# Kernel optimization log

Measured on AMD Instinct MI355X. Metric: run time of the kernel, lower is better.

## Reference

```python
import jax, jax.numpy as jnp
import numpy as np

B, OBS, N, HEADS, SIZE, HID = 8192, 512, 8, 5, 64, 1024
SUM = HEADS * SIZE  # sum(per_robot_dims) = 320
NEG = -1.0e9


def setup_inputs() -> dict:
    key = jax.random.key(0)
    ks = jax.random.split(key, 12)
    init = lambda k, sh, fan: (jax.random.normal(k, sh, jnp.float32) / np.sqrt(fan)).astype(jnp.float32)
    obs = jax.random.normal(ks[0], (B, OBS), jnp.float32)
    actions = jax.random.randint(ks[1], (B, N * HEADS), 0, SIZE)
    masks = jax.random.randint(ks[2], (B, N, HEADS, SIZE), 0, 2).astype(jnp.int32)
    return {
        "obs": obs,
        "actions": actions,
        "masks": masks,
        "W1": init(ks[3], (OBS, HID), OBS), "b1": jnp.zeros((HID,), jnp.float32),
        "W2": init(ks[4], (HID, HID), HID), "b2": jnp.zeros((HID,), jnp.float32),
        "headsW": init(ks[5], (N, HID, SUM), HID), "headsb": jnp.zeros((N, SUM), jnp.float32),
        "Wc1": init(ks[6], (HID, HID // 2), HID), "bc1": jnp.zeros((HID // 2,), jnp.float32),
        "Wc2": init(ks[7], (HID // 2, 1), HID // 2), "bc2": jnp.zeros((1,), jnp.float32),
    }


def reference(obs, actions, masks, W1, b1, W2, b2, headsW, headsb, Wc1, bc1, Wc2, bc2):
    # Shared encoder: two Linear+ReLU layers.
    h = jax.nn.relu(obs @ W1 + b1)
    h = jax.nn.relu(h @ W2 + b2)  # [B, HID]
    # Per-robot heads, batched into one einsum: [B, N, SUM]
    logits = jnp.einsum('bh,nhs->bns', h, headsW) + headsb
    seg = logits.reshape(B, N, HEADS, SIZE)
    # Masked softmax: invalid entries set to -1e9 (matches seg[~mask] = -1e9).
    seg = jnp.where(masks.astype(bool), seg, NEG)
    logp = jax.nn.log_softmax(seg, axis=-1)          # [B, N, HEADS, SIZE]
    probs = jnp.exp(logp)
    acts = actions.reshape(B, N, HEADS)
    lp_terms = jnp.take_along_axis(logp, acts[..., None], axis=-1)[..., 0]
    ent_terms = -jnp.sum(probs * logp, axis=-1)
    # Out-of-range action -> log-prob -1000 and no entropy contribution.
    valid = acts < SIZE
    logps = jnp.where(valid, lp_terms, -1000.0).sum(axis=(1, 2))
    entropy = jnp.where(valid, ent_terms, 0.0).sum(axis=(1, 2))
    # Critic value head.
    values = (jax.nn.relu(h @ Wc1 + bc1) @ Wc2 + bc2)[..., 0]
    return logps, entropy, values
```

## Files before the change

### kernel.cpp

```cpp
#include <hip/hip_runtime.h>
#include <hip/hip_bf16.h>
#include <stdint.h>


typedef __bf16 v8bf __attribute__((ext_vector_type(8)));
typedef float  v4f  __attribute__((ext_vector_type(4)));

__device__ __forceinline__ void load_lds16(const void* g, void* l) {
  auto gp = (const __attribute__((address_space(1))) char*)(uintptr_t)g;
  auto lp = (__attribute__((address_space(3))) char*)(uintptr_t)l;
  __builtin_amdgcn_global_load_lds(gp, lp, 16, 0, 0);
}


__global__ void convert_obs(const float4* __restrict__ in, int4* __restrict__ out, int n8) {
  const int i = blockIdx.x * blockDim.x + threadIdx.x;
  if (i >= n8) return;
  const float4 x = in[i * 2], y = in[i * 2 + 1];
  union { __hip_bfloat16 h[8]; int4 v; } u;
  u.h[0] = __float2bfloat16(x.x);
  u.h[1] = __float2bfloat16(x.y);
  u.h[2] = __float2bfloat16(x.z);
  u.h[3] = __float2bfloat16(x.w);
  u.h[4] = __float2bfloat16(y.x);
  u.h[5] = __float2bfloat16(y.y);
  u.h[6] = __float2bfloat16(y.z);
  u.h[7] = __float2bfloat16(y.w);
  out[i] = u.v;
}

__global__ void build_bias(const float* __restrict__ headsb, const float* __restrict__ bc1,
                           float* __restrict__ biasc) {
  const int i = blockIdx.x * blockDim.x + threadIdx.x;
  if (i < 2560) biasc[i] = headsb[i];
  else if (i < 3072) biasc[i] = bc1[i - 2560];
}

__global__ void transpose_to_bf16(const float* __restrict__ in, __hip_bfloat16* __restrict__ out,
                                  int R, int C) {
  __shared__ float t[32][33];
  const int bx = blockIdx.x * 32, by = blockIdx.y * 32;
  in  += (size_t)blockIdx.z * R * C;
  out += (size_t)blockIdx.z * R * C;
  const int x = threadIdx.x, y = threadIdx.y;
#pragma unroll
  for (int i = 0; i < 32; i += 8)
    t[y + i][x] = in[(size_t)(by + y + i) * C + bx + x];
  __syncthreads();
#pragma unroll
  for (int i = 0; i < 32; i += 8)
    out[(size_t)(bx + y + i) * R + by + x] = __float2bfloat16(t[x][y + i]);
}


__global__ __launch_bounds__(256, 2)
void gemm_bf16_tn(const __hip_bfloat16* __restrict__ A,
                  const __hip_bfloat16* __restrict__ Bt,
                  const float* __restrict__ bias,
                  __hip_bfloat16* __restrict__ C,
                  int M, int N, int K, int relu_from) {
  __shared__ char As[8192];
  __shared__ char Bs[8192];
  const int tid  = threadIdx.x;
  const int lane = tid & 63;
  const int wave = tid >> 6;
  const int wr = wave >> 1, wc = wave & 1;
  const int m0 = blockIdx.y * 128, n0 = blockIdx.x * 128;

  const int c0 = tid, c1 = tid + 256;
  const int r0 = ((c0 >> 3) << 1) | (((c0 >> 2) ^ (c0 >> 4)) & 1);
  const int s0 = (c0 & 3) ^ (r0 & 3);
  const int r1 = ((c1 >> 3) << 1) | (((c1 >> 2) ^ (c1 >> 4)) & 1);
  const int s1 = (c1 & 3) ^ (r1 & 3);

  const char* pa0 = (const char*)A  + ((size_t)(m0 + r0) * K) * 2 + s0 * 16;
  const char* pa1 = (const char*)A  + ((size_t)(m0 + r1) * K) * 2 + s1 * 16;
  const char* pb0 = (const char*)Bt + ((size_t)(n0 + r0) * K) * 2 + s0 * 16;
  const char* pb1 = (const char*)Bt + ((size_t)(n0 + r1) * K) * 2 + s1 * 16;

  char* la0 = As + c0 * 16;
  char* la1 = As + c1 * 16;
  char* lb0 = Bs + c0 * 16;
  char* lb1 = Bs + c1 * 16;

  const int lr = lane & 15, ls = lane >> 4;
  int offA[4], offB[4];
#pragma unroll
  for (int m = 0; m < 4; ++m) {
    const int rA = wr * 64 + m * 16 + lr;
    offA[m] = ((rA * 4 + (ls ^ (rA & 3))) ^ (rA & 4)) * 16;
    const int rB = wc * 64 + m * 16 + lr;
    offB[m] = ((rB * 4 + (ls ^ (rB & 3))) ^ (rB & 4)) * 16;
  }

  v4f acc[4][4] = {};

  const int nk = K >> 5;
  for (int it = 0; it < nk; ++it) {
    load_lds16(pa0, la0);
    load_lds16(pa1, la1);
    load_lds16(pb0, lb0);
    load_lds16(pb1, lb1);
    pa0 += 64; pa1 += 64; pb0 += 64; pb1 += 64;
    __syncthreads();

    v8bf av[4], bvv[4];
#pragma unroll
    for (int m = 0; m < 4; ++m) av[m]  = *(const v8bf*)(As + offA[m]);
#pragma unroll
    for (int n = 0; n < 4; ++n) bvv[n] = *(const v8bf*)(Bs + offB[n]);
#pragma unroll
    for (int m = 0; m < 4; ++m)
#pragma unroll
      for (int n = 0; n < 4; ++n)
        acc[m][n] = __builtin_amdgcn_mfma_f32_16x16x32_bf16(av[m], bvv[n], acc[m][n], 0, 0, 0);
    __syncthreads();
  }

  const int colb = n0 + wc * 64 + lr;
  const int rowb = m0 + wr * 64 + ls * 4;
#pragma unroll
  for (int n = 0; n < 4; ++n) {
    const int col = colb + n * 16;
    const float bv = bias[col];
    const bool rl = (col >= relu_from);
#pragma unroll
    for (int m = 0; m < 4; ++m) {
      const int rbase = rowb + m * 16;
#pragma unroll
      for (int j = 0; j < 4; ++j) {
        float v = acc[m][n][j] + bv;
        if (rl) v = fmaxf(v, 0.0f);
        C[(size_t)(rbase + j) * N + col] = __float2bfloat16(v);
      }
    }
  }
}


__global__ __launch_bounds__(256)
void finalize_kernel(const __hip_bfloat16* __restrict__ out3,
                     const int* __restrict__ masks,
                     const int* __restrict__ actions,
                     const float* __restrict__ Wc2,
                     const float* __restrict__ bc2,
                     float* __restrict__ out) {
  const int lane = threadIdx.x & 63;
  const int r = blockIdx.x * 4 + (threadIdx.x >> 6);
  const __hip_bfloat16* row = out3 + (size_t)r * 3072;
  const int* mrow = masks + (size_t)r * 2560;
  const int* arow = actions + r * 40;

  const int g = lane >> 3;
  const int gl = lane & 7;

  float lp_sum = 0.f, ent_sum = 0.f;

#pragma unroll
  for (int p = 0; p < 5; ++p) {
    const int base = p * 512 + lane * 8;
    union { int4 q; __hip_bfloat16 h[8]; } u;
    u.q = *(const int4*)(row + base);
    const int4 ma = *(const int4*)(mrow + base);
    const int4 mb = *(const int4*)(mrow + base + 4);

    float v[8];
    v[0] = ma.x ? __bfloat162float(u.h[0]) : -1.0e9f;
    v[1] = ma.y ? __bfloat162float(u.h[1]) : -1.0e9f;
    v[2] = ma.z ? __bfloat162float(u.h[2]) : -1.0e9f;
    v[3] = ma.w ? __bfloat162float(u.h[3]) : -1.0e9f;
    v[4] = mb.x ? __bfloat162float(u.h[4]) : -1.0e9f;
    v[5] = mb.y ? __bfloat162float(u.h[5]) : -1.0e9f;
    v[6] = mb.z ? __bfloat162float(u.h[6]) : -1.0e9f;
    v[7] = mb.w ? __bfloat162float(u.h[7]) : -1.0e9f;

    float mx = fmaxf(fmaxf(fmaxf(v[0], v[1]), fmaxf(v[2], v[3])),
                     fmaxf(fmaxf(v[4], v[5]), fmaxf(v[6], v[7])));
#pragma unroll
    for (int o = 1; o < 8; o <<= 1) mx = fmaxf(mx, __shfl_xor(mx, o));

    float s = 0.f, sv = 0.f;
#pragma unroll
    for (int j = 0; j < 8; ++j) {
      const float e = __expf(v[j] - mx);
      s += e;
      sv += e * v[j];
    }
#pragma unroll
    for (int o = 1; o < 8; o <<= 1) { s += __shfl_xor(s, o); sv += __shfl_xor(sv, o); }

    const float logZ = __logf(s) + mx;

    const int act = arow[p * 8 + g];
    float va_loc = v[0];
#pragma unroll
    for (int j = 1; j < 8; ++j) va_loc = ((act & 7) == j) ? v[j] : va_loc;
    const float va = __shfl(va_loc, (lane & 56) | ((act >> 3) & 7));

    if ((unsigned)act < 64u) {
      lp_sum += va - logZ;
      ent_sum += logZ - sv / s;
    } else {
      lp_sum += -1000.0f;
    }
  }

#pragma unroll
  for (int o = 8; o < 64; o <<= 1) {
    lp_sum += __shfl_xor(lp_sum, o);
    ent_sum += __shfl_xor(ent_sum, o);
  }

  union { int4 q; __hip_bfloat16 h[8]; } c;
  c.q = *(const int4*)(row + 2560 + lane * 8);
  const float4 w0 = *(const float4*)(Wc2 + lane * 8);
  const float4 w1 = *(const float4*)(Wc2 + lane * 8 + 4);
  float acc = __bfloat162float(c.h[0]) * w0.x + __bfloat162float(c.h[1]) * w0.y +
              __bfloat162float(c.h[2]) * w0.z + __bfloat162float(c.h[3]) * w0.w +
              __bfloat162float(c.h[4]) * w1.x + __bfloat162float(c.h[5]) * w1.y +
              __bfloat162float(c.h[6]) * w1.z + __bfloat162float(c.h[7]) * w1.w;
#pragma unroll
  for (int o = 32; o > 0; o >>= 1) acc += __shfl_xor(acc, o);

  if (lane == 0) {
    out[r]         = lp_sum;
    out[8192 + r]  = ent_sum;
    out[16384 + r] = acc + bc2[0];
  }
}


extern "C" void kernel_launch(void* const* d_in, const int* in_sizes, int n_in,
                              void* d_out, int out_size, void* d_ws, size_t ws_size,
                              hipStream_t stream) {
  const float* obs    = (const float*)d_in[0];
  const int*   actions= (const int*)d_in[1];
  const int*   masks  = (const int*)d_in[2];
  const float* W1     = (const float*)d_in[3];
  const float* b1     = (const float*)d_in[4];
  const float* W2     = (const float*)d_in[5];
  const float* b2     = (const float*)d_in[6];
  const float* headsW = (const float*)d_in[7];
  const float* headsb = (const float*)d_in[8];
  const float* Wc1    = (const float*)d_in[9];
  const float* bc1    = (const float*)d_in[10];
  const float* Wc2    = (const float*)d_in[11];
  const float* bc2    = (const float*)d_in[12];
  float* out = (float*)d_out;

  char* ws = (char*)d_ws;
  __hip_bfloat16* obsB  = (__hip_bfloat16*)(ws);
  __hip_bfloat16* W1t   = (__hip_bfloat16*)(ws + 8388608);
  __hip_bfloat16* W2t   = (__hip_bfloat16*)(ws + 9437184);
  __hip_bfloat16* Wbigt = (__hip_bfloat16*)(ws + 11534336);
  float*          biasc = (float*)(ws + 17825792);
  __hip_bfloat16* h1    = (__hip_bfloat16*)(ws + 17838080);
  __hip_bfloat16* h2    = (__hip_bfloat16*)(ws + 34615296);
  __hip_bfloat16* out3  = (__hip_bfloat16*)(ws + 51392512);

  convert_obs<<<2048, 256, 0, stream>>>((const float4*)obs, (int4*)obsB, 524288);
  build_bias<<<12, 256, 0, stream>>>(headsb, bc1, biasc);
  transpose_to_bf16<<<dim3(32, 16, 1), dim3(32, 8), 0, stream>>>(W1, W1t, 512, 1024);
  transpose_to_bf16<<<dim3(32, 32, 1), dim3(32, 8), 0, stream>>>(W2, W2t, 1024, 1024);
  transpose_to_bf16<<<dim3(10, 32, 8), dim3(32, 8), 0, stream>>>(headsW, Wbigt, 1024, 320);
  transpose_to_bf16<<<dim3(16, 32, 1), dim3(32, 8), 0, stream>>>(Wc1, Wbigt + 2560 * 1024, 1024, 512);

  gemm_bf16_tn<<<dim3(8, 64), 256, 0, stream>>>(obsB, W1t, b1, h1, 8192, 1024, 512, 0);
  gemm_bf16_tn<<<dim3(8, 64), 256, 0, stream>>>(h1, W2t, b2, h2, 8192, 1024, 1024, 0);
  gemm_bf16_tn<<<dim3(24, 64), 256, 0, stream>>>(h2, Wbigt, biasc, out3, 8192, 3072, 1024, 2560);

  finalize_kernel<<<2048, 256, 0, stream>>>(out3, masks, actions, Wc2, bc2, out);
}
```

Measured before the change: 154.3 us.

## Replace GEMM with 256x256-tile double-buffered 8-phase pipelined kernel

Swaps the simple 128x128, single-buffer, K=32-per-step GEMM for a 512-thread kernel that computes 256x256 output tiles with K=128 steps. Global-to-LDS loads are double buffered and interleaved with MFMA phases using explicit waitcnt, barriers, sched_barrier and setprio. Block IDs are remapped across 8 groups to spread tiles over XCDs. The goal is to hide memory latency and raise data reuse per tile, at the cost of 128KB of LDS, more registers and fewer blocks (128/384), which risks poor CU occupancy on the smaller GEMMs.

```diff
diff --git a/kernel.cpp b/kernel.cpp
--- a/kernel.cpp
+++ b/kernel.cpp
@@ -53,79 +53,190 @@
 }
 
 
-__global__ __launch_bounds__(256, 2)
-void gemm_bf16_tn(const __hip_bfloat16* __restrict__ A,
-                  const __hip_bfloat16* __restrict__ Bt,
-                  const float* __restrict__ bias,
-                  __hip_bfloat16* __restrict__ C,
-                  int M, int N, int K, int relu_from) {
-  __shared__ char As[8192];
-  __shared__ char Bs[8192];
+__device__ __forceinline__ void rd_a(v8bf (&a)[4][2], const char* base, int mbase) {
+#pragma unroll
+  for (int m = 0; m < 4; ++m)
+#pragma unroll
+    for (int ks = 0; ks < 2; ++ks)
+      a[m][ks] = *(const v8bf*)(base + (((mbase + m) * 2 + ks) << 10));
+}
+
+__device__ __forceinline__ void rd_b2(v8bf (&b)[4][2], const char* base, int n0) {
+#pragma unroll
+  for (int n = 0; n < 2; ++n)
+#pragma unroll
+    for (int ks = 0; ks < 2; ++ks)
+      b[n0 + n][ks] = *(const v8bf*)(base + (((n0 + n) * 2 + ks) << 10));
+}
+
+template<int M0, int N0>
+__device__ __forceinline__ void mfma_quad(v4f (&acc)[8][4], const v8bf (&a)[4][2],
+                                          const v8bf (&b)[4][2]) {
+#pragma unroll
+  for (int m = 0; m < 4; ++m)
+#pragma unroll
+    for (int n = 0; n < 2; ++n)
+#pragma unroll
+      for (int ks = 0; ks < 2; ++ks)
+        acc[M0 + m][N0 + n] =
+            __builtin_amdgcn_mfma_f32_16x16x32_bf16(a[m][ks], b[N0 + n][ks],
+                                                    acc[M0 + m][N0 + n], 0, 0, 0);
+}
+
+#define BARRIER __builtin_amdgcn_s_barrier()
+#define SCHEDB  __builtin_amdgcn_sched_barrier(0)
+#define WAIT_LGKM0 do { asm volatile("s_waitcnt lgkmcnt(0)" ::: "memory"); SCHEDB; } while (0)
+#define WAIT_VM2   do { asm volatile("s_waitcnt vmcnt(2)" ::: "memory"); SCHEDB; } while (0)
+#define WAIT_VM0   do { asm volatile("s_waitcnt vmcnt(0)" ::: "memory"); SCHEDB; } while (0)
+
+#define MFMA_PH(Q) do { __builtin_amdgcn_s_setprio(1); Q; __builtin_amdgcn_s_setprio(0); SCHEDB; } while (0)
+
+#define ST_A0(db) { load_lds16(pA0a, s0 + ((db) << 16));          load_lds16(pA0b, s0 + ((db) << 16) + 8192);  pA0a += 128; pA0b += 128; }
+#define ST_A1(db) { load_lds16(pA1a, s0 + ((db) << 16) + 16384);  load_lds16(pA1b, s0 + ((db) << 16) + 24576); pA1a += 128; pA1b += 128; }
+#define ST_B0(db) { load_lds16(pB0a, s0 + ((db) << 16) + 32768);  load_lds16(pB0b, s0 + ((db) << 16) + 40960); pB0a += 128; pB0b += 128; }
+#define ST_B1(db) { load_lds16(pB1a, s0 + ((db) << 16) + 49152);  load_lds16(pB1b, s0 + ((db) << 16) + 57344); pB1a += 128; pB1b += 128; }
+
+__global__ __launch_bounds__(512, 2)
+void gemm_8ph(const __hip_bfloat16* __restrict__ A,
+              const __hip_bfloat16* __restrict__ Bt,
+              const float* __restrict__ bias,
+              __hip_bfloat16* __restrict__ C,
+              int M, int N, int K, int relu_from, int gx) {
+  __shared__ char smem[131072];
+
   const int tid  = threadIdx.x;
   const int lane = tid & 63;
   const int wave = tid >> 6;
-  const int wr = wave >> 1, wc = wave & 1;
-  const int m0 = blockIdx.y * 128, n0 = blockIdx.x * 128;
-
-  const int c0 = tid, c1 = tid + 256;
-  const int r0 = ((c0 >> 3) << 1) | (((c0 >> 2) ^ (c0 >> 4)) & 1);
-  const int s0 = (c0 & 3) ^ (r0 & 3);
-  const int r1 = ((c1 >> 3) << 1) | (((c1 >> 2) ^ (c1 >> 4)) & 1);
-  const int s1 = (c1 & 3) ^ (r1 & 3);
-
-  const char* pa0 = (const char*)A  + ((size_t)(m0 + r0) * K) * 2 + s0 * 16;
-  const char* pa1 = (const char*)A  + ((size_t)(m0 + r1) * K) * 2 + s1 * 16;
-  const char* pb0 = (const char*)Bt + ((size_t)(n0 + r0) * K) * 2 + s0 * 16;
-  const char* pb1 = (const char*)Bt + ((size_t)(n0 + r1) * K) * 2 + s1 * 16;
-
-  char* la0 = As + c0 * 16;
-  char* la1 = As + c1 * 16;
-  char* lb0 = Bs + c0 * 16;
-  char* lb1 = Bs + c1 * 16;
-
+  const int wr = wave >> 2;
+  const int wc = wave & 3;
   const int lr = lane & 15, ls = lane >> 4;
-  int offA[4], offB[4];
-#pragma unroll
-  for (int m = 0; m < 4; ++m) {
-    const int rA = wr * 64 + m * 16 + lr;
-    offA[m] = ((rA * 4 + (ls ^ (rA & 3))) ^ (rA & 4)) * 16;
-    const int rB = wc * 64 + m * 16 + lr;
-    offB[m] = ((rB * 4 + (ls ^ (rB & 3))) ^ (rB & 4)) * 16;
-  }
-
-  v4f acc[4][4] = {};
-
-  const int nk = K >> 5;
-  for (int it = 0; it < nk; ++it) {
-    load_lds16(pa0, la0);
-    load_lds16(pa1, la1);
-    load_lds16(pb0, lb0);
-    load_lds16(pb1, lb1);
-    pa0 += 64; pa1 += 64; pb0 += 64; pb1 += 64;
-    __syncthreads();
-
-    v8bf av[4], bvv[4];
-#pragma unroll
-    for (int m = 0; m < 4; ++m) av[m]  = *(const v8bf*)(As + offA[m]);
-#pragma unroll
-    for (int n = 0; n < 4; ++n) bvv[n] = *(const v8bf*)(Bs + offB[n]);
-#pragma unroll
-    for (int m = 0; m < 4; ++m)
-#pragma unroll
-      for (int n = 0; n < 4; ++n)
-        acc[m][n] = __builtin_amdgcn_mfma_f32_16x16x32_bf16(av[m], bvv[n], acc[m][n], 0, 0, 0);
-    __syncthreads();
-  }
+
+  const int nwg = gridDim.x;
+  const int q8 = nwg >> 3;
+  const int id = (blockIdx.x & 7) * q8 + (blockIdx.x >> 3);
+  const int bx = id % gx, by = id / gx;
+  const int m0 = by * 256, n0 = bx * 256;
+
+  const int o0 = tid << 4;
+  const int s_0 = o0 ^ (((o0 >> 9) & 1) << 5);
+  const int r0 = ((s_0 >> 10) >> 1) * 16 + ((s_0 >> 6) & 15);
+  const int cb0 = (((((s_0 >> 10) & 1) << 2) | ((s_0 >> 4) & 3)) << 4);
+  const int o1 = (tid + 512) << 4;
+  const int s_1 = o1 ^ (((o1 >> 9) & 1) << 5);
+  const int r1 = ((s_1 >> 10) >> 1) * 16 + ((s_1 >> 6) & 15);
+  const int cb1 = (((((s_1 >> 10) & 1) << 2) | ((s_1 >> 4) & 3)) << 4);
+
+  const size_t K2 = (size_t)K * 2;
+  const char* pA0a = (const char*)A + (size_t)(m0 +       r0) * K2 + cb0;
+  const char* pA0b = (const char*)A + (size_t)(m0 +       r1) * K2 + cb1;
+  const char* pA1a = (const char*)A + (size_t)(m0 + 128 + r0) * K2 + cb0;
+  const char* pA1b = (const char*)A + (size_t)(m0 + 128 + r1) * K2 + cb1;
+  const char* pB0a = (const char*)Bt + (size_t)(n0 +       r0) * K2 + cb0;
+  const char* pB0b = (const char*)Bt + (size_t)(n0 +       r1) * K2 + cb1;
+  const char* pB1a = (const char*)Bt + (size_t)(n0 + 128 + r0) * K2 + cb0;
+  const char* pB1b = (const char*)Bt + (size_t)(n0 + 128 + r1) * K2 + cb1;
+
+  char* const s0 = smem + (tid << 4);
+
+  const int laneOff = lr * 64 + ((ls * 16) ^ ((lr & 8) << 2));
+  const char* aB0 = smem + wr * 16384 + laneOff;
+  const char* bB0 = smem + 32768 + (wc >> 1) * 16384 + (wc & 1) * 8192 + laneOff;
+  const char* aB1 = aB0 + 65536;
+  const char* bB1 = bB0 + 65536;
+
+  v4f acc[8][4] = {};
+  v8bf aLo[4][2], aHi[4][2], bFr[4][2];
+
+  ST_A0(0); ST_A1(0); ST_B0(0); ST_B1(0);
+  ST_A0(1);
+  WAIT_VM2;
+  BARRIER; SCHEDB;
+
+  const int NI = (K >> 7) - 1;
+  for (int i = 0; i < NI; ++i) {
+    rd_a(aLo, aB0, 0); rd_b2(bFr, bB0, 0);
+    ST_A1(1);
+    BARRIER; WAIT_LGKM0;
+    MFMA_PH((mfma_quad<0, 0>(acc, aLo, bFr)));
+    BARRIER;
+    rd_b2(bFr, bB0, 2);
+    ST_B0(1);
+    BARRIER; WAIT_LGKM0;
+    MFMA_PH((mfma_quad<0, 2>(acc, aLo, bFr)));
+    BARRIER;
+    rd_a(aHi, aB0, 4);
+    ST_B1(1);
+    BARRIER; WAIT_LGKM0;
+    MFMA_PH((mfma_quad<4, 2>(acc, aHi, bFr)));
+    BARRIER;
+    ST_A0(0);
+    WAIT_VM2;
+    BARRIER;
+    MFMA_PH((mfma_quad<4, 0>(acc, aHi, bFr)));
+    BARRIER;
+    rd_a(aLo, aB1, 0); rd_b2(bFr, bB1, 0);
+    ST_A1(0);
+    BARRIER; WAIT_LGKM0;
+    MFMA_PH((mfma_quad<0, 0>(acc, aLo, bFr)));
+    BARRIER;
+    rd_b2(bFr, bB1, 2);
+    ST_B0(0);
+    BARRIER; WAIT_LGKM0;
+    MFMA_PH((mfma_quad<0, 2>(acc, aLo, bFr)));
+    BARRIER;
+    rd_a(aHi, aB1, 4);
+    ST_B1(0);
+    BARRIER; WAIT_LGKM0;
+    MFMA_PH((mfma_quad<4, 2>(acc, aHi, bFr)));
+    BARRIER;
+    ST_A0(1);
+    WAIT_VM2;
+    BARRIER;
+    MFMA_PH((mfma_quad<4, 0>(acc, aHi, bFr)));
+    BARRIER;
+  }
+
+  rd_a(aLo, aB0, 0); rd_b2(bFr, bB0, 0);
+  ST_A1(1);
+  BARRIER; WAIT_LGKM0;
+  MFMA_PH((mfma_quad<0, 0>(acc, aLo, bFr)));
+  BARRIER;
+  rd_b2(bFr, bB0, 2);
+  ST_B0(1);
+  BARRIER; WAIT_LGKM0;
+  MFMA_PH((mfma_quad<0, 2>(acc, aLo, bFr)));
+  BARRIER;
+  rd_a(aHi, aB0, 4);
+  ST_B1(1);
+  BARRIER; WAIT_LGKM0;
+  MFMA_PH((mfma_quad<4, 2>(acc, aHi, bFr)));
+  BARRIER;
+  WAIT_VM0;
+  BARRIER;
+  MFMA_PH((mfma_quad<4, 0>(acc, aHi, bFr)));
+  BARRIER;
+  rd_a(aLo, aB1, 0); rd_b2(bFr, bB1, 0);
+  BARRIER; WAIT_LGKM0;
+  MFMA_PH((mfma_quad<0, 0>(acc, aLo, bFr)));
+  BARRIER;
+  rd_b2(bFr, bB1, 2);
+  BARRIER; WAIT_LGKM0;
+  MFMA_PH((mfma_quad<0, 2>(acc, aLo, bFr)));
+  BARRIER;
+  rd_a(aHi, aB1, 4);
+  BARRIER; WAIT_LGKM0;
+  MFMA_PH((mfma_quad<4, 2>(acc, aHi, bFr)));
+  MFMA_PH((mfma_quad<4, 0>(acc, aHi, bFr)));
 
   const int colb = n0 + wc * 64 + lr;
-  const int rowb = m0 + wr * 64 + ls * 4;
+  const int rowb = m0 + wr * 128 + ls * 4;
 #pragma unroll
   for (int n = 0; n < 4; ++n) {
     const int col = colb + n * 16;
     const float bv = bias[col];
     const bool rl = (col >= relu_from);
 #pragma unroll
-    for (int m = 0; m < 4; ++m) {
+    for (int m = 0; m < 8; ++m) {
       const int rbase = rowb + m * 16;
 #pragma unroll
       for (int j = 0; j < 4; ++j) {
@@ -152,7 +263,6 @@
   const int* arow = actions + r * 40;
 
   const int g = lane >> 3;
-  const int gl = lane & 7;
 
   float lp_sum = 0.f, ent_sum = 0.f;
 
@@ -265,9 +375,9 @@
   transpose_to_bf16<<<dim3(10, 32, 8), dim3(32, 8), 0, stream>>>(headsW, Wbigt, 1024, 320);
   transpose_to_bf16<<<dim3(16, 32, 1), dim3(32, 8), 0, stream>>>(Wc1, Wbigt + 2560 * 1024, 1024, 512);
 
-  gemm_bf16_tn<<<dim3(8, 64), 256, 0, stream>>>(obsB, W1t, b1, h1, 8192, 1024, 512, 0);
-  gemm_bf16_tn<<<dim3(8, 64), 256, 0, stream>>>(h1, W2t, b2, h2, 8192, 1024, 1024, 0);
-  gemm_bf16_tn<<<dim3(24, 64), 256, 0, stream>>>(h2, Wbigt, biasc, out3, 8192, 3072, 1024, 2560);
+  gemm_8ph<<<dim3(128), 512, 0, stream>>>(obsB, W1t, b1, h1, 8192, 1024, 512, 0, 4);
+  gemm_8ph<<<dim3(128), 512, 0, stream>>>(h1, W2t, b2, h2, 8192, 1024, 1024, 0, 4);
+  gemm_8ph<<<dim3(384), 512, 0, stream>>>(h2, Wbigt, biasc, out3, 8192, 3072, 1024, 2560, 12);
 
   finalize_kernel<<<2048, 256, 0, stream>>>(out3, masks, actions, Wc2, bc2, out);
 }
```

Result: slower. 159.8 us (+3.5%).

## Replace bf16 GEMM with 4-stage pipelined, larger-tile 512-thread kernel

Applied to the files above, without the earlier changes.

Replaces the single-buffered 128x128 GEMM with a templated kernel that uses 256-row tiles, 8 waves, and a 4-deep LDS ring. Global-to-LDS loads are issued several k-steps ahead, with explicit vmcnt and lgkmcnt waits and raw barriers, so memory latency can overlap the MFMA work. It also remaps block IDs across 8 groups to improve cache locality, and raises wave priority around the MFMA bursts. The cost is much larger LDS use per block, which may limit occupancy to one block per CU, and more fragile hand-written synchronisation.

```diff
diff --git a/kernel.cpp b/kernel.cpp
--- a/kernel.cpp
+++ b/kernel.cpp
@@ -10,6 +10,20 @@
   auto gp = (const __attribute__((address_space(1))) char*)(uintptr_t)g;
   auto lp = (__attribute__((address_space(3))) char*)(uintptr_t)l;
   __builtin_amdgcn_global_load_lds(gp, lp, 16, 0, 0);
+}
+
+#define BARRIER __builtin_amdgcn_s_barrier()
+#define SCHEDB  __builtin_amdgcn_sched_barrier(0)
+#define WAIT_LGKM0 do { asm volatile("s_waitcnt lgkmcnt(0)" ::: "memory"); SCHEDB; } while (0)
+
+template<int N>
+__device__ __forceinline__ void wait_vm() {
+  if constexpr (N == 8)      asm volatile("s_waitcnt vmcnt(8)" ::: "memory");
+  else if constexpr (N == 6) asm volatile("s_waitcnt vmcnt(6)" ::: "memory");
+  else if constexpr (N == 4) asm volatile("s_waitcnt vmcnt(4)" ::: "memory");
+  else if constexpr (N == 3) asm volatile("s_waitcnt vmcnt(3)" ::: "memory");
+  else                       asm volatile("s_waitcnt vmcnt(0)" ::: "memory");
+  SCHEDB;
 }
 
 
@@ -53,79 +67,133 @@
 }
 
 
-__global__ __launch_bounds__(256, 2)
-void gemm_bf16_tn(const __hip_bfloat16* __restrict__ A,
-                  const __hip_bfloat16* __restrict__ Bt,
-                  const float* __restrict__ bias,
-                  __hip_bfloat16* __restrict__ C,
-                  int M, int N, int K, int relu_from) {
-  __shared__ char As[8192];
-  __shared__ char Bs[8192];
+__device__ __forceinline__ void decode_chunk(int o, int& r, int& cb) {
+  const int L = o ^ (((o >> 9) & 1) << 5);
+  r  = ((L >> 10) << 4) | ((L >> 6) & 15);
+  cb = ((L >> 4) & 3) << 4;
+}
+
+template<int WM>
+__global__ __launch_bounds__(512, 2)
+void gemm_kt(const __hip_bfloat16* __restrict__ A,
+             const __hip_bfloat16* __restrict__ Bt,
+             const float* __restrict__ bias,
+             __hip_bfloat16* __restrict__ C,
+             int N, int K, int relu_from, int gx) {
+  constexpr int WN   = 8 / WM;
+  constexpr int MR   = 16 / WM;
+  constexpr int BREG = WN * 4096;
+  constexpr int TB   = 16384 + BREG;
+  constexpr int NSTG = 2 + WN / 2;
+
+  __shared__ char smem[4 * TB];
+
   const int tid  = threadIdx.x;
   const int lane = tid & 63;
   const int wave = tid >> 6;
-  const int wr = wave >> 1, wc = wave & 1;
-  const int m0 = blockIdx.y * 128, n0 = blockIdx.x * 128;
-
-  const int c0 = tid, c1 = tid + 256;
-  const int r0 = ((c0 >> 3) << 1) | (((c0 >> 2) ^ (c0 >> 4)) & 1);
-  const int s0 = (c0 & 3) ^ (r0 & 3);
-  const int r1 = ((c1 >> 3) << 1) | (((c1 >> 2) ^ (c1 >> 4)) & 1);
-  const int s1 = (c1 & 3) ^ (r1 & 3);
-
-  const char* pa0 = (const char*)A  + ((size_t)(m0 + r0) * K) * 2 + s0 * 16;
-  const char* pa1 = (const char*)A  + ((size_t)(m0 + r1) * K) * 2 + s1 * 16;
-  const char* pb0 = (const char*)Bt + ((size_t)(n0 + r0) * K) * 2 + s0 * 16;
-  const char* pb1 = (const char*)Bt + ((size_t)(n0 + r1) * K) * 2 + s1 * 16;
-
-  char* la0 = As + c0 * 16;
-  char* la1 = As + c1 * 16;
-  char* lb0 = Bs + c0 * 16;
-  char* lb1 = Bs + c1 * 16;
-
+  const int wr = wave / WN, wc = wave % WN;
   const int lr = lane & 15, ls = lane >> 4;
-  int offA[4], offB[4];
-#pragma unroll
-  for (int m = 0; m < 4; ++m) {
-    const int rA = wr * 64 + m * 16 + lr;
-    offA[m] = ((rA * 4 + (ls ^ (rA & 3))) ^ (rA & 4)) * 16;
-    const int rB = wc * 64 + m * 16 + lr;
-    offB[m] = ((rB * 4 + (ls ^ (rB & 3))) ^ (rB & 4)) * 16;
-  }
-
-  v4f acc[4][4] = {};
-
-  const int nk = K >> 5;
-  for (int it = 0; it < nk; ++it) {
-    load_lds16(pa0, la0);
-    load_lds16(pa1, la1);
-    load_lds16(pb0, lb0);
-    load_lds16(pb1, lb1);
-    pa0 += 64; pa1 += 64; pb0 += 64; pb1 += 64;
-    __syncthreads();
-
-    v8bf av[4], bvv[4];
-#pragma unroll
-    for (int m = 0; m < 4; ++m) av[m]  = *(const v8bf*)(As + offA[m]);
-#pragma unroll
-    for (int n = 0; n < 4; ++n) bvv[n] = *(const v8bf*)(Bs + offB[n]);
+
+  const int nwg = gridDim.x;
+  const int q8 = nwg >> 3;
+  const int id = (blockIdx.x & 7) * q8 + (blockIdx.x >> 3);
+  const int bx = id % gx, by = id / gx;
+  const int m0 = by * 256, n0 = bx * (WN * 64);
+
+  int rA0, cA0, rA1, cA1, rB0, cB0, rB1, cB1;
+  decode_chunk(tid * 16, rA0, cA0);
+  decode_chunk(tid * 16 + 8192, rA1, cA1);
+  decode_chunk(tid * 16, rB0, cB0);
+  decode_chunk(tid * 16 + 8192, rB1, cB1);
+
+  const size_t K2 = (size_t)K * 2;
+  const char* pA0 = (const char*)A + (size_t)(m0 + rA0) * K2 + cA0;
+  const char* pA1 = (const char*)A + (size_t)(m0 + rA1) * K2 + cA1;
+  const char* pB0 = (const char*)Bt + (size_t)(n0 + rB0) * K2 + cB0;
+  const char* pB1 = (const char*)Bt + (size_t)(n0 + rB1) * K2 + cB1;
+
+  char* const s0 = smem + (tid << 4);
+
+  const int laneOff = lr * 64 + ((ls * 16) ^ ((lr & 8) << 2));
+
+  v4f acc[MR][4] = {};
+
+  auto stage_A = [&](int stOff) {
+    load_lds16(pA0, s0 + stOff);
+    load_lds16(pA1, s0 + stOff + 8192);
+    pA0 += 64; pA1 += 64;
+  };
+  auto stage_B = [&](int stOff) {
+    load_lds16(pB0, s0 + stOff + 16384);
+    pB0 += 64;
+    if constexpr (WN == 4) {
+      load_lds16(pB1, s0 + stOff + 24576);
+      pB1 += 64;
+    }
+  };
+
+  auto tile = [&](int bufOff, int stOff, bool doStage, auto gate) {
+    const char* aB = smem + bufOff + wr * (MR * 1024) + laneOff;
+    const char* bB = smem + bufOff + 16384 + wc * 4096 + laneOff;
+    v8bf af[4], bfr[4];
+#pragma unroll
+    for (int m = 0; m < 4; ++m) af[m] = *(const v8bf*)(aB + m * 1024);
+#pragma unroll
+    for (int n = 0; n < 4; ++n) bfr[n] = *(const v8bf*)(bB + n * 1024);
+    if (doStage) {
+      stage_A(stOff);
+      if constexpr (MR == 4) stage_B(stOff);
+    }
+    BARRIER; WAIT_LGKM0;
+    __builtin_amdgcn_s_setprio(1);
 #pragma unroll
     for (int m = 0; m < 4; ++m)
 #pragma unroll
       for (int n = 0; n < 4; ++n)
-        acc[m][n] = __builtin_amdgcn_mfma_f32_16x16x32_bf16(av[m], bvv[n], acc[m][n], 0, 0, 0);
-    __syncthreads();
-  }
+        acc[m][n] = __builtin_amdgcn_mfma_f32_16x16x32_bf16(af[m], bfr[n], acc[m][n], 0, 0, 0);
+    __builtin_amdgcn_s_setprio(0); SCHEDB;
+    if constexpr (MR == 8) {
+      BARRIER;
+#pragma unroll
+      for (int m = 0; m < 4; ++m) af[m] = *(const v8bf*)(aB + (4 + m) * 1024);
+      if (doStage) stage_B(stOff);
+      BARRIER; WAIT_LGKM0;
+      __builtin_amdgcn_s_setprio(1);
+#pragma unroll
+      for (int m = 0; m < 4; ++m)
+#pragma unroll
+        for (int n = 0; n < 4; ++n)
+          acc[4 + m][n] =
+              __builtin_amdgcn_mfma_f32_16x16x32_bf16(af[m], bfr[n], acc[4 + m][n], 0, 0, 0);
+      __builtin_amdgcn_s_setprio(0); SCHEDB;
+    }
+    gate();
+    BARRIER;
+  };
+
+  stage_A(0);      stage_B(0);
+  stage_A(TB);     stage_B(TB);
+  stage_A(2 * TB); stage_B(2 * TB);
+  wait_vm<2 * NSTG>();
+  BARRIER; SCHEDB;
+
+  const int NT = K >> 5;
+  int t = 0;
+  for (; t + 3 < NT; ++t)
+    tile((t & 3) * TB, ((t + 3) & 3) * TB, true, [] { wait_vm<2 * NSTG>(); });
+  tile((t & 3) * TB, 0, false, [] { wait_vm<NSTG>(); }); ++t;
+  tile((t & 3) * TB, 0, false, [] { wait_vm<0>(); });    ++t;
+  tile((t & 3) * TB, 0, false, [] {});
 
   const int colb = n0 + wc * 64 + lr;
-  const int rowb = m0 + wr * 64 + ls * 4;
+  const int rowb = m0 + wr * (MR * 16) + ls * 4;
 #pragma unroll
   for (int n = 0; n < 4; ++n) {
     const int col = colb + n * 16;
     const float bv = bias[col];
     const bool rl = (col >= relu_from);
 #pragma unroll
-    for (int m = 0; m < 4; ++m) {
+    for (int m = 0; m < MR; ++m) {
       const int rbase = rowb + m * 16;
 #pragma unroll
       for (int j = 0; j < 4; ++j) {
@@ -152,7 +220,6 @@
   const int* arow = actions + r * 40;
 
   const int g = lane >> 3;
-  const int gl = lane & 7;
 
   float lp_sum = 0.f, ent_sum = 0.f;
 
@@ -265,9 +332,9 @@
   transpose_to_bf16<<<dim3(10, 32, 8), dim3(32, 8), 0, stream>>>(headsW, Wbigt, 1024, 320);
   transpose_to_bf16<<<dim3(16, 32, 1), dim3(32, 8), 0, stream>>>(Wc1, Wbigt + 2560 * 1024, 1024, 512);
 
-  gemm_bf16_tn<<<dim3(8, 64), 256, 0, stream>>>(obsB, W1t, b1, h1, 8192, 1024, 512, 0);
-  gemm_bf16_tn<<<dim3(8, 64), 256, 0, stream>>>(h1, W2t, b2, h2, 8192, 1024, 1024, 0);
-  gemm_bf16_tn<<<dim3(24, 64), 256, 0, stream>>>(h2, Wbigt, biasc, out3, 8192, 3072, 1024, 2560);
+  gemm_kt<4><<<dim3(256), 512, 0, stream>>>(obsB, W1t, b1, h1, 1024, 512, 0, 8);
+  gemm_kt<4><<<dim3(256), 512, 0, stream>>>(h1, W2t, b2, h2, 1024, 1024, 0, 8);
+  gemm_kt<2><<<dim3(384), 512, 0, stream>>>(h2, Wbigt, biasc, out3, 3072, 1024, 2560, 12);
 
   finalize_kernel<<<2048, 256, 0, stream>>>(out3, masks, actions, Wc2, bc2, out);
 }
```

After: 150.3 us. 2.6% less time.

## Double-buffer GEMM LDS tiles with BK=64 and XCD-aware block remap

Applied to the files above, without the earlier changes.

Replaces the single-buffered BK=32 GEMM with a double-buffered BK=64 version in a 64KB LDS allocation. Global-to-LDS loads for the next tile are issued while the MFMAs of the current tile run, using explicit waitcnt, barriers and setprio. It also remaps the 1D block index so that consecutive tiles spread across the XCDs, and changes the LDS swizzle. The aim is to hide global load latency and halve the barriers per K step, at the cost of more LDS per block, which may lower occupancy below 2 blocks per CU.

```diff
diff --git a/kernel.cpp b/kernel.cpp
--- a/kernel.cpp
+++ b/kernel.cpp
@@ -11,6 +11,13 @@
   auto lp = (__attribute__((address_space(3))) char*)(uintptr_t)l;
   __builtin_amdgcn_global_load_lds(gp, lp, 16, 0, 0);
 }
+
+#define BARRIER __builtin_amdgcn_s_barrier()
+#define SCHEDB  __builtin_amdgcn_sched_barrier(0)
+#define WAIT_LGKM0 do { asm volatile("s_waitcnt lgkmcnt(0)" ::: "memory"); SCHEDB; } while (0)
+#define WAIT_LGKM8 do { asm volatile("s_waitcnt lgkmcnt(8)" ::: "memory"); SCHEDB; } while (0)
+#define WAIT_VM8   do { asm volatile("s_waitcnt vmcnt(8)" ::: "memory"); SCHEDB; } while (0)
+#define WAIT_VM0   do { asm volatile("s_waitcnt vmcnt(0)" ::: "memory"); SCHEDB; } while (0)
 
 
 __global__ void convert_obs(const float4* __restrict__ in, int4* __restrict__ out, int n8) {
@@ -53,69 +60,106 @@
 }
 
 
+__device__ __forceinline__ void decode_chunk(int o, int& r, int& cb) {
+  const int L = o ^ (((o >> 9) & 1) << 5);
+  r  = ((L >> 10) << 4) | ((L >> 6) & 15);
+  cb = ((L >> 4) & 3) << 4;
+}
+
 __global__ __launch_bounds__(256, 2)
-void gemm_bf16_tn(const __hip_bfloat16* __restrict__ A,
-                  const __hip_bfloat16* __restrict__ Bt,
-                  const float* __restrict__ bias,
-                  __hip_bfloat16* __restrict__ C,
-                  int M, int N, int K, int relu_from) {
-  __shared__ char As[8192];
-  __shared__ char Bs[8192];
+void gemm_db(const __hip_bfloat16* __restrict__ A,
+             const __hip_bfloat16* __restrict__ Bt,
+             const float* __restrict__ bias,
+             __hip_bfloat16* __restrict__ C,
+             int N, int K, int relu_from, int gx) {
+  __shared__ char smem[65536];
+
   const int tid  = threadIdx.x;
   const int lane = tid & 63;
   const int wave = tid >> 6;
   const int wr = wave >> 1, wc = wave & 1;
-  const int m0 = blockIdx.y * 128, n0 = blockIdx.x * 128;
-
-  const int c0 = tid, c1 = tid + 256;
-  const int r0 = ((c0 >> 3) << 1) | (((c0 >> 2) ^ (c0 >> 4)) & 1);
-  const int s0 = (c0 & 3) ^ (r0 & 3);
-  const int r1 = ((c1 >> 3) << 1) | (((c1 >> 2) ^ (c1 >> 4)) & 1);
-  const int s1 = (c1 & 3) ^ (r1 & 3);
-
-  const char* pa0 = (const char*)A  + ((size_t)(m0 + r0) * K) * 2 + s0 * 16;
-  const char* pa1 = (const char*)A  + ((size_t)(m0 + r1) * K) * 2 + s1 * 16;
-  const char* pb0 = (const char*)Bt + ((size_t)(n0 + r0) * K) * 2 + s0 * 16;
-  const char* pb1 = (const char*)Bt + ((size_t)(n0 + r1) * K) * 2 + s1 * 16;
-
-  char* la0 = As + c0 * 16;
-  char* la1 = As + c1 * 16;
-  char* lb0 = Bs + c0 * 16;
-  char* lb1 = Bs + c1 * 16;
-
   const int lr = lane & 15, ls = lane >> 4;
-  int offA[4], offB[4];
-#pragma unroll
-  for (int m = 0; m < 4; ++m) {
-    const int rA = wr * 64 + m * 16 + lr;
-    offA[m] = ((rA * 4 + (ls ^ (rA & 3))) ^ (rA & 4)) * 16;
-    const int rB = wc * 64 + m * 16 + lr;
-    offB[m] = ((rB * 4 + (ls ^ (rB & 3))) ^ (rB & 4)) * 16;
-  }
+
+  const int nwg = gridDim.x;
+  const int q8 = nwg >> 3;
+  const int id = (blockIdx.x & 7) * q8 + (blockIdx.x >> 3);
+  const int bx = id % gx, by = id / gx;
+  const int m0 = by * 128, n0 = bx * 128;
+
+  int r0, c0, r1, c1;
+  decode_chunk(tid * 16, r0, c0);
+  decode_chunk(tid * 16 + 4096, r1, c1);
+
+  const size_t K2 = (size_t)K * 2;
+  const char* pA0 = (const char*)A  + (size_t)(m0 + r0) * K2 + c0;
+  const char* pA1 = (const char*)A  + (size_t)(m0 + r1) * K2 + c1;
+  const char* pB0 = (const char*)Bt + (size_t)(n0 + r0) * K2 + c0;
+  const char* pB1 = (const char*)Bt + (size_t)(n0 + r1) * K2 + c1;
+
+  char* const s0 = smem + (tid << 4);
+
+  auto stage = [&](int buf) {
+    char* d = s0 + (buf << 15);
+    load_lds16(pA0,      d);
+    load_lds16(pA1,      d + 4096);
+    load_lds16(pA0 + 64, d + 8192);
+    load_lds16(pA1 + 64, d + 12288);
+    load_lds16(pB0,      d + 16384);
+    load_lds16(pB1,      d + 20480);
+    load_lds16(pB0 + 64, d + 24576);
+    load_lds16(pB1 + 64, d + 28672);
+    pA0 += 128; pA1 += 128; pB0 += 128; pB1 += 128;
+  };
+
+  const int laneOff = lr * 64 + ((ls * 16) ^ ((lr & 8) << 2));
 
   v4f acc[4][4] = {};
 
-  const int nk = K >> 5;
-  for (int it = 0; it < nk; ++it) {
-    load_lds16(pa0, la0);
-    load_lds16(pa1, la1);
-    load_lds16(pb0, lb0);
-    load_lds16(pb1, lb1);
-    pa0 += 64; pa1 += 64; pb0 += 64; pb1 += 64;
-    __syncthreads();
-
-    v8bf av[4], bvv[4];
-#pragma unroll
-    for (int m = 0; m < 4; ++m) av[m]  = *(const v8bf*)(As + offA[m]);
-#pragma unroll
-    for (int n = 0; n < 4; ++n) bvv[n] = *(const v8bf*)(Bs + offB[n]);
+  auto tile = [&](int buf, bool doStage, auto gate) {
+    const char* aB = smem + (buf << 15) + wr * 4096 + laneOff;
+    const char* bB = smem + (buf << 15) + 16384 + wc * 4096 + laneOff;
+    v8bf a0[4], b0[4], a1[4], b1[4];
+#pragma unroll
+    for (int m = 0; m < 4; ++m) a0[m] = *(const v8bf*)(aB + m * 1024);
+#pragma unroll
+    for (int n = 0; n < 4; ++n) b0[n] = *(const v8bf*)(bB + n * 1024);
+#pragma unroll
+    for (int m = 0; m < 4; ++m) a1[m] = *(const v8bf*)(aB + 8192 + m * 1024);
+#pragma unroll
+    for (int n = 0; n < 4; ++n) b1[n] = *(const v8bf*)(bB + 8192 + n * 1024);
+    WAIT_LGKM8;
+    __builtin_amdgcn_s_setprio(1);
 #pragma unroll
     for (int m = 0; m < 4; ++m)
 #pragma unroll
       for (int n = 0; n < 4; ++n)
-        acc[m][n] = __builtin_amdgcn_mfma_f32_16x16x32_bf16(av[m], bvv[n], acc[m][n], 0, 0, 0);
-    __syncthreads();
-  }
+        acc[m][n] = __builtin_amdgcn_mfma_f32_16x16x32_bf16(a0[m], b0[n], acc[m][n], 0, 0, 0);
+    __builtin_amdgcn_s_setprio(0); SCHEDB;
+    WAIT_LGKM0;
+    BARRIER;
+    if (doStage) stage(buf);
+    __builtin_amdgcn_s_setprio(1);
+#pragma unroll
+    for (int m = 0; m < 4; ++m)
+#pragma unroll
+      for (int n = 0; n < 4; ++n)
+        acc[m][n] = __builtin_amdgcn_mfma_f32_16x16x32_bf16(a1[m], b1[n], acc[m][n], 0, 0, 0);
+    __builtin_amdgcn_s_setprio(0); SCHEDB;
+    gate();
+    BARRIER;
+  };
+
+  stage(0);
+  stage(1);
+  WAIT_VM8;
+  BARRIER; SCHEDB;
+
+  const int NT = K >> 6;
+  int t = 0;
+  for (; t < NT - 2; ++t)
+    tile(t & 1, true, [] { WAIT_VM8; });
+  tile(t & 1, false, [] { WAIT_VM0; }); ++t;
+  tile(t & 1, false, [] {});
 
   const int colb = n0 + wc * 64 + lr;
   const int rowb = m0 + wr * 64 + ls * 4;
@@ -152,7 +196,6 @@
   const int* arow = actions + r * 40;
 
   const int g = lane >> 3;
-  const int gl = lane & 7;
 
   float lp_sum = 0.f, ent_sum = 0.f;
 
@@ -265,9 +308,9 @@
   transpose_to_bf16<<<dim3(10, 32, 8), dim3(32, 8), 0, stream>>>(headsW, Wbigt, 1024, 320);
   transpose_to_bf16<<<dim3(16, 32, 1), dim3(32, 8), 0, stream>>>(Wc1, Wbigt + 2560 * 1024, 1024, 512);
 
-  gemm_bf16_tn<<<dim3(8, 64), 256, 0, stream>>>(obsB, W1t, b1, h1, 8192, 1024, 512, 0);
-  gemm_bf16_tn<<<dim3(8, 64), 256, 0, stream>>>(h1, W2t, b2, h2, 8192, 1024, 1024, 0);
-  gemm_bf16_tn<<<dim3(24, 64), 256, 0, stream>>>(h2, Wbigt, biasc, out3, 8192, 3072, 1024, 2560);
+  gemm_db<<<dim3(512), 256, 0, stream>>>(obsB, W1t, b1, h1, 1024, 512, 0, 8);
+  gemm_db<<<dim3(512), 256, 0, stream>>>(h1, W2t, b2, h2, 1024, 1024, 0, 8);
+  gemm_db<<<dim3(1536), 256, 0, stream>>>(h2, Wbigt, biasc, out3, 3072, 1024, 2560, 24);
 
   finalize_kernel<<<2048, 256, 0, stream>>>(out3, masks, actions, Wc2, bc2, out);
 }
```

Result: faster. 137.9 us (-10.6%).
